# Optimization experiments

Hardware: AMD Instinct MI355X
Metric: run time of the kernel (lower is better)

The kernel has to match this reference:

```python
import jax, jax.numpy as jnp
import numpy as np

DILATIONS = [1, 2, 4, 8, 16, 32, 64, 128, 256, 512]
C = 256   # channels
K = 3     # kernel size


def causal_conv(x, w, b, d):
    # x: [B, C_in, T], w: [C_out, C_in, K] -> [B, C_out, T], left-padded causal
    y = jax.lax.conv_general_dilated(
        x, w,
        window_strides=(1,),
        padding=[((K - 1) * d, 0)],
        rhs_dilation=(d,),
        dimension_numbers=('NCH', 'OIH', 'NCH'))
    return y + b[None, :, None]


def setup_inputs() -> dict:
    key = jax.random.key(0)
    ks = jax.random.split(key, 5)
    L = len(DILATIONS)
    B, T = 4, 8192
    s = 0.05  # weight scale
    return {
        'input': jax.random.normal(ks[0], (B, C, T), jnp.float32),
        'weights_conv': jax.random.normal(ks[1], (L, 2 * C, C, K), jnp.float32) * s,
        'biases_conv': jax.random.normal(ks[2], (L, 2 * C), jnp.float32) * s,
        'weights_out': jax.random.normal(ks[3], (L, C, C), jnp.float32) * s,
        'biases_out': jax.random.normal(ks[4], (L, C), jnp.float32) * s,
    }


def reference(input, weights_conv, biases_conv, weights_out, biases_out):
    x = input  # [B, C, T]
    L = len(DILATIONS)
    skips = []
    for i, d in enumerate(DILATIONS):
        z = causal_conv(x, weights_conv[i], biases_conv[i], d)  # [B, 2C, T]
        # gated activation: tanh on first half, sigmoid on second half
        h = jnp.tanh(z[:, :C]) * jax.nn.sigmoid(z[:, C:])       # [B, C, T]
        skips.append(h)
        if i < L - 1:
            # 1x1 output transform (disabled on the last layer)
            out = jnp.einsum('oc,bct->bot', weights_out[i], h) + biases_out[i][None, :, None]
        else:
            out = h
        x = out + x  # residual connection applied in the stack
    return x, jnp.stack(skips, axis=0)  # ([B,C,T], [L,B,C,T])
```

## Files before the change

### kernel.cpp

```cpp
#include <hip/hip_runtime.h>
#include <hip/hip_bf16.h>

#define BATCH 4
#define CCH 256
#define TLEN 8192
#define LAYERS 10
#define BCT (BATCH*CCH*TLEN)
#define TPAD 1024
#define TROWS (TPAD + TLEN)

typedef __attribute__((ext_vector_type(8))) short bf16x8;
typedef __attribute__((ext_vector_type(4))) float f32x4;

__device__ __forceinline__ unsigned short f2b(float f) {
  union { float f; unsigned u; } v; v.f = f;
  unsigned r = (v.u + 0x7FFFu + ((v.u >> 16) & 1u)) >> 16;
  return (unsigned short)r;
}
__device__ __forceinline__ float b2f(unsigned short h) {
  union { unsigned u; float f; } v; v.u = ((unsigned)h) << 16;
  return v.f;
}

__device__ __forceinline__ void gload16(const void* g, void* l) {
  __builtin_amdgcn_global_load_lds((__attribute__((address_space(1))) void*)g,
                                   (__attribute__((address_space(3))) void*)l, 16, 0, 0);
}

__device__ __forceinline__ float fast_tanh(float x) {
  float a = fabsf(x);
  float e = __expf(-2.f * a);
  float th = (1.f - e) * __builtin_amdgcn_rcpf(1.f + e);
  return copysignf(th, x);
}
__device__ __forceinline__ float fast_sigmoid(float x) {
  return __builtin_amdgcn_rcpf(1.f + __expf(-x));
}

__global__ void repack_w(const float* __restrict__ wc, const float* __restrict__ wo,
                         unsigned short* __restrict__ Wb, unsigned short* __restrict__ Wob) {
  size_t g = (size_t)blockIdx.x * 256 + threadIdx.x;
  const size_t NA = (size_t)LAYERS * 3 * 4 * 128 * 256;
  if (g < NA) {
    int c   = (int)(g & 255);
    int row = (int)((g >> 8) & 127);
    int y   = (int)((g >> 15) & 3);
    int lt  = (int)(g >> 17);
    int tap = lt % 3, l = lt / 3;
    int ch = y * 64 + ((row >> 5) << 4) + (row & 15) + (((row >> 4) & 1) << 8);
    Wb[g] = f2b(wc[(((size_t)l * 512 + ch) * 256 + c) * 3 + tap]);
  } else {
    size_t g2 = g - NA;
    if (g2 < (size_t)LAYERS * 256 * 256) Wob[g2] = f2b(wo[g2]);
  }
}

__global__ void zero_pads(unsigned short* __restrict__ xTb) {
  size_t off = (size_t)blockIdx.y * TROWS * CCH;
  int i = blockIdx.x * 256 + threadIdx.x;
  ulonglong2 z; z.x = 0ull; z.y = 0ull;
  ((ulonglong2*)(xTb + off))[i] = z;
}

__global__ void transpose_in(const float* __restrict__ in, float* __restrict__ xT,
                             unsigned short* __restrict__ xTb) {
  __shared__ float tile[32][33];
  const int tid = threadIdx.x;
  const int t0 = blockIdx.x * 32, c0 = blockIdx.y * 32, b = blockIdx.z;
#pragma unroll
  for (int q = 0; q < 4; ++q) {
    int e = tid + 256 * q; int r = e >> 5, cc = e & 31;
    tile[r][cc] = in[((size_t)b * CCH + c0 + r) * TLEN + t0 + cc];
  }
  __syncthreads();
#pragma unroll
  for (int q = 0; q < 4; ++q) {
    int e = tid + 256 * q; int r = e >> 5, cc = e & 31;
    float v = tile[cc][r];
    xT[((size_t)b * TLEN + t0 + r) * CCH + c0 + cc] = v;
    xTb[((size_t)b * TROWS + TPAD + t0 + r) * CCH + c0 + cc] = f2b(v);
  }
}

__global__ void final_addT(const float* __restrict__ xT, const unsigned short* __restrict__ hT,
                           float* __restrict__ out) {
  __shared__ float tile[32][33];
  const int tid = threadIdx.x;
  const int t0 = blockIdx.x * 32, c0 = blockIdx.y * 32, b = blockIdx.z;
#pragma unroll
  for (int q = 0; q < 4; ++q) {
    int e = tid + 256 * q; int r = e >> 5, cc = e & 31;
    size_t idx = ((size_t)b * TLEN + t0 + r) * CCH + c0 + cc;
    tile[r][cc] = xT[idx] + b2f(hT[idx]);
  }
  __syncthreads();
#pragma unroll
  for (int q = 0; q < 4; ++q) {
    int e = tid + 256 * q; int r = e >> 5, cc = e & 31;
    out[((size_t)b * CCH + c0 + r) * TLEN + t0 + cc] = tile[cc][r];
  }
}

__global__ __launch_bounds__(256)
void conv_gate_kernel(const unsigned short* __restrict__ xTb,
                      const unsigned short* __restrict__ Wl,
                      const float* __restrict__ bias,
                      unsigned short* __restrict__ hT,
                      float* __restrict__ skip,
                      int d) {
  __shared__ unsigned short As[128 * 32];
  __shared__ unsigned short Bs[128 * 32];

  const int tid  = threadIdx.x;
  const int lane = tid & 63;
  const int wv   = tid >> 6;
  const int wm   = wv & 1, wn = wv >> 1;
  const int col  = lane & 15, quad = lane >> 4;

  const int t0 = blockIdx.x * 128;
  const int y  = blockIdx.y;
  const int o0 = y * 64;
  const int b  = blockIdx.z;

  const int rl = lane >> 2;
  const int kl = (lane & 3) * 8;
  const int ch0 = wv * 2;

  f32x4 acc[4][4];
  const f32x4 zero = {0.f, 0.f, 0.f, 0.f};
#pragma unroll
  for (int i = 0; i < 4; ++i)
#pragma unroll
    for (int j = 0; j < 4; ++j) acc[i][j] = zero;

  for (int tap = 0; tap < 3; ++tap) {
    const int s = (2 - tap) * d;
    const unsigned short* Ab = xTb + ((size_t)b * TROWS + TPAD + t0 - s) * CCH;
    const unsigned short* Wb = Wl + ((size_t)tap * 4 + y) * 128 * 256;
    for (int c0 = 0; c0 < 256; c0 += 32) {
      __syncthreads();
      gload16(Ab + (size_t)(ch0 * 16      + rl) * CCH + c0 + kl, &As[ ch0      * 512]);
      gload16(Ab + (size_t)(ch0 * 16 + 16 + rl) * CCH + c0 + kl, &As[(ch0 + 1) * 512]);
      gload16(Wb + (size_t)(ch0 * 16      + rl) * 256 + c0 + kl, &Bs[ ch0      * 512]);
      gload16(Wb + (size_t)(ch0 * 16 + 16 + rl) * 256 + c0 + kl, &Bs[(ch0 + 1) * 512]);
      __syncthreads();
      const int k0 = quad * 8;
      bf16x8 af[4], bfv[4];
#pragma unroll
      for (int mf = 0; mf < 4; ++mf)
        af[mf] = *(const bf16x8*)&As[(wm * 64 + mf * 16 + col) * 32 + k0];
#pragma unroll
      for (int nf = 0; nf < 4; ++nf)
        bfv[nf] = *(const bf16x8*)&Bs[(wn * 64 + nf * 16 + col) * 32 + k0];
#pragma unroll
      for (int mf = 0; mf < 4; ++mf)
#pragma unroll
        for (int nf = 0; nf < 4; ++nf)
          acc[mf][nf] = __builtin_amdgcn_mfma_f32_16x16x32_bf16(af[mf], bfv[nf], acc[mf][nf], 0, 0, 0);
    }
  }

#pragma unroll
  for (int mf = 0; mf < 4; ++mf) {
    const int tb = t0 + wm * 64 + mf * 16 + quad * 4;
#pragma unroll
    for (int p = 0; p < 2; ++p) {
      const int pair = wn * 2 + p;
      const int ch = o0 + pair * 16 + col;
      const float btop = bias[ch];
      const float bbot = bias[ch + 256];
      f32x4 zt = acc[mf][2 * p];
      f32x4 zb = acc[mf][2 * p + 1];
      float hr[4];
#pragma unroll
      for (int r = 0; r < 4; ++r) {
        float h = fast_tanh(zt[r] + btop) * fast_sigmoid(zb[r] + bbot);
        hr[r] = h;
        hT[((size_t)b * TLEN + tb + r) * CCH + ch] = f2b(h);
      }
      float4 hv; hv.x = hr[0]; hv.y = hr[1]; hv.z = hr[2]; hv.w = hr[3];
      *(float4*)&skip[((size_t)b * CCH + ch) * TLEN + tb] = hv;
    }
  }
}

__global__ __launch_bounds__(256)
void onexone_kernel(const unsigned short* __restrict__ hT,
                    const unsigned short* __restrict__ Wo,
                    const float* __restrict__ bias,
                    float* __restrict__ xT,
                    unsigned short* __restrict__ xTb) {
  __shared__ unsigned short As[128 * 32];
  __shared__ unsigned short Bs[128 * 32];

  const int tid  = threadIdx.x;
  const int lane = tid & 63;
  const int wv   = tid >> 6;
  const int wm   = wv & 1, wn = wv >> 1;
  const int col  = lane & 15, quad = lane >> 4;

  const int t0 = blockIdx.x * 128;
  const int o0 = blockIdx.y * 128;
  const int b  = blockIdx.z;

  const int rl = lane >> 2;
  const int kl = (lane & 3) * 8;
  const int ch0 = wv * 2;

  const unsigned short* Ab = hT + (size_t)b * TLEN * CCH + (size_t)t0 * CCH;
  const unsigned short* Wb = Wo + (size_t)o0 * 256;

  f32x4 acc[4][4];
  const f32x4 zero = {0.f, 0.f, 0.f, 0.f};
#pragma unroll
  for (int i = 0; i < 4; ++i)
#pragma unroll
    for (int j = 0; j < 4; ++j) acc[i][j] = zero;

  for (int c0 = 0; c0 < 256; c0 += 32) {
    __syncthreads();
    gload16(Ab + (size_t)(ch0 * 16      + rl) * CCH + c0 + kl, &As[ ch0      * 512]);
    gload16(Ab + (size_t)(ch0 * 16 + 16 + rl) * CCH + c0 + kl, &As[(ch0 + 1) * 512]);
    gload16(Wb + (size_t)(ch0 * 16      + rl) * 256 + c0 + kl, &Bs[ ch0      * 512]);
    gload16(Wb + (size_t)(ch0 * 16 + 16 + rl) * 256 + c0 + kl, &Bs[(ch0 + 1) * 512]);
    __syncthreads();
    const int k0 = quad * 8;
    bf16x8 af[4], bfv[4];
#pragma unroll
    for (int mf = 0; mf < 4; ++mf)
      af[mf] = *(const bf16x8*)&As[(wm * 64 + mf * 16 + col) * 32 + k0];
#pragma unroll
    for (int nf = 0; nf < 4; ++nf)
      bfv[nf] = *(const bf16x8*)&Bs[(wn * 64 + nf * 16 + col) * 32 + k0];
#pragma unroll
    for (int mf = 0; mf < 4; ++mf)
#pragma unroll
      for (int nf = 0; nf < 4; ++nf)
        acc[mf][nf] = __builtin_amdgcn_mfma_f32_16x16x32_bf16(af[mf], bfv[nf], acc[mf][nf], 0, 0, 0);
  }

#pragma unroll
  for (int mf = 0; mf < 4; ++mf) {
    const int tb = t0 + wm * 64 + mf * 16 + quad * 4;
#pragma unroll
    for (int nf = 0; nf < 4; ++nf) {
      const int ch = o0 + wn * 64 + nf * 16 + col;
      const float bo = bias[ch];
#pragma unroll
      for (int r = 0; r < 4; ++r) {
        size_t idx = ((size_t)b * TLEN + tb + r) * CCH + ch;
        float nv = xT[idx] + acc[mf][nf][r] + bo;
        xT[idx] = nv;
        xTb[((size_t)b * TROWS + TPAD + tb + r) * CCH + ch] = f2b(nv);
      }
    }
  }
}

extern "C" void kernel_launch(void* const* d_in, const int* in_sizes, int n_in,
                              void* d_out, int out_size, void* d_ws, size_t ws_size,
                              hipStream_t stream) {
  const float* input = (const float*)d_in[0];
  const float* wconv = (const float*)d_in[1];
  const float* bconv = (const float*)d_in[2];
  const float* wout  = (const float*)d_in[3];
  const float* bout  = (const float*)d_in[4];
  float* out   = (float*)d_out;
  float* skips = out + (size_t)BCT;

  char* ws = (char*)d_ws;
  float*          xT  = (float*)ws;
  unsigned short* xTb = (unsigned short*)(ws + (size_t)BCT * 4);
  unsigned short* hT  = (unsigned short*)(ws + (size_t)BCT * 4
                                             + (size_t)BATCH * TROWS * CCH * 2);
  unsigned short* Wb  = hT + (size_t)BCT;
  unsigned short* Wob = Wb + (size_t)LAYERS * 3 * 512 * 256;

  static const int dil[LAYERS] = {1, 2, 4, 8, 16, 32, 64, 128, 256, 512};

  repack_w<<<17920, 256, 0, stream>>>(wconv, wout, Wb, Wob);
  zero_pads<<<dim3(128, BATCH), 256, 0, stream>>>(xTb);
  transpose_in<<<dim3(TLEN / 32, CCH / 32, BATCH), 256, 0, stream>>>(input, xT, xTb);

  for (int l = 0; l < LAYERS; ++l) {
    conv_gate_kernel<<<dim3(TLEN / 128, 4, BATCH), 256, 0, stream>>>(
        xTb, Wb + (size_t)l * 3 * 512 * 256, bconv + (size_t)l * 512,
        hT, skips + (size_t)l * BCT, dil[l]);
    if (l < LAYERS - 1) {
      onexone_kernel<<<dim3(TLEN / 128, 2, BATCH), 256, 0, stream>>>(
          hT, Wob + (size_t)l * 256 * 256, bout + (size_t)l * 256, xT, xTb);
    } else {
      final_addT<<<dim3(TLEN / 32, CCH / 32, BATCH), 256, 0, stream>>>(xT, hT, out);
    }
  }
}
```

Before: 1.045 ms.

## Double-buffer LDS tiles in conv and 1x1 GEMM kernels

Both the dilated-conv gate kernel and the 1x1 output kernel now use two LDS buffers. The next K-chunk is issued (flattened over taps and channel chunks) while MFMAs run on the current one, which removes one barrier per iteration. This is meant to hide global-to-LDS load latency behind compute. In exchange, LDS use per block doubles, which may reduce occupancy, and whether the overlap happens depends on how gload16 completes.

```diff
diff --git a/kernel.cpp b/kernel.cpp
--- a/kernel.cpp
+++ b/kernel.cpp
@@ -108,8 +108,8 @@
                       unsigned short* __restrict__ hT,
                       float* __restrict__ skip,
                       int d) {
-  __shared__ unsigned short As[128 * 32];
-  __shared__ unsigned short Bs[128 * 32];
+  __shared__ unsigned short As[2][128 * 32];
+  __shared__ unsigned short Bs[2][128 * 32];
 
   const int tid  = threadIdx.x;
   const int lane = tid & 63;
@@ -126,6 +126,8 @@
   const int kl = (lane & 3) * 8;
   const int ch0 = wv * 2;
 
+  const unsigned short* Arow = xTb + ((size_t)b * TROWS + TPAD + t0) * CCH;
+
   f32x4 acc[4][4];
   const f32x4 zero = {0.f, 0.f, 0.f, 0.f};
 #pragma unroll
@@ -133,31 +135,42 @@
 #pragma unroll
     for (int j = 0; j < 4; ++j) acc[i][j] = zero;
 
-  for (int tap = 0; tap < 3; ++tap) {
-    const int s = (2 - tap) * d;
-    const unsigned short* Ab = xTb + ((size_t)b * TROWS + TPAD + t0 - s) * CCH;
-    const unsigned short* Wb = Wl + ((size_t)tap * 4 + y) * 128 * 256;
-    for (int c0 = 0; c0 < 256; c0 += 32) {
-      __syncthreads();
-      gload16(Ab + (size_t)(ch0 * 16      + rl) * CCH + c0 + kl, &As[ ch0      * 512]);
-      gload16(Ab + (size_t)(ch0 * 16 + 16 + rl) * CCH + c0 + kl, &As[(ch0 + 1) * 512]);
-      gload16(Wb + (size_t)(ch0 * 16      + rl) * 256 + c0 + kl, &Bs[ ch0      * 512]);
-      gload16(Wb + (size_t)(ch0 * 16 + 16 + rl) * 256 + c0 + kl, &Bs[(ch0 + 1) * 512]);
-      __syncthreads();
-      const int k0 = quad * 8;
-      bf16x8 af[4], bfv[4];
-#pragma unroll
-      for (int mf = 0; mf < 4; ++mf)
-        af[mf] = *(const bf16x8*)&As[(wm * 64 + mf * 16 + col) * 32 + k0];
+  const int NCHUNK = 24;
+
+  auto stage = [&](int idx, int buf) {
+    const int tap = idx >> 3;
+    const int c0  = (idx & 7) << 5;
+    const unsigned short* Ab = Arow - (size_t)((2 - tap) * d) * CCH;
+    const unsigned short* Wb = Wl + ((size_t)tap * 4 + y) * (128 * 256);
+    gload16(Ab + (size_t)(ch0 * 16      + rl) * CCH + c0 + kl, &As[buf][ ch0      * 512]);
+    gload16(Ab + (size_t)(ch0 * 16 + 16 + rl) * CCH + c0 + kl, &As[buf][(ch0 + 1) * 512]);
+    gload16(Wb + (size_t)(ch0 * 16      + rl) * 256 + c0 + kl, &Bs[buf][ ch0      * 512]);
+    gload16(Wb + (size_t)(ch0 * 16 + 16 + rl) * 256 + c0 + kl, &Bs[buf][(ch0 + 1) * 512]);
+  };
+
+  auto step = [&](int buf, int next_idx) {
+    const int k0 = quad * 8;
+    bf16x8 af[4], bfv[4];
+#pragma unroll
+    for (int mf = 0; mf < 4; ++mf)
+      af[mf] = *(const bf16x8*)&As[buf][(wm * 64 + mf * 16 + col) * 32 + k0];
+#pragma unroll
+    for (int nf = 0; nf < 4; ++nf)
+      bfv[nf] = *(const bf16x8*)&Bs[buf][(wn * 64 + nf * 16 + col) * 32 + k0];
+    if (next_idx < NCHUNK) stage(next_idx, buf ^ 1);
+#pragma unroll
+    for (int mf = 0; mf < 4; ++mf)
 #pragma unroll
       for (int nf = 0; nf < 4; ++nf)
-        bfv[nf] = *(const bf16x8*)&Bs[(wn * 64 + nf * 16 + col) * 32 + k0];
-#pragma unroll
-      for (int mf = 0; mf < 4; ++mf)
-#pragma unroll
-        for (int nf = 0; nf < 4; ++nf)
-          acc[mf][nf] = __builtin_amdgcn_mfma_f32_16x16x32_bf16(af[mf], bfv[nf], acc[mf][nf], 0, 0, 0);
-    }
+        acc[mf][nf] = __builtin_amdgcn_mfma_f32_16x16x32_bf16(af[mf], bfv[nf], acc[mf][nf], 0, 0, 0);
+  };
+
+  stage(0, 0);
+  __syncthreads();
+#pragma unroll 1
+  for (int i = 0; i < NCHUNK; i += 2) {
+    step(0, i + 1); __syncthreads();
+    step(1, i + 2); __syncthreads();
   }
 
 #pragma unroll
@@ -190,8 +203,8 @@
                     const float* __restrict__ bias,
                     float* __restrict__ xT,
                     unsigned short* __restrict__ xTb) {
-  __shared__ unsigned short As[128 * 32];
-  __shared__ unsigned short Bs[128 * 32];
+  __shared__ unsigned short As[2][128 * 32];
+  __shared__ unsigned short Bs[2][128 * 32];
 
   const int tid  = threadIdx.x;
   const int lane = tid & 63;
@@ -217,26 +230,39 @@
 #pragma unroll
     for (int j = 0; j < 4; ++j) acc[i][j] = zero;
 
-  for (int c0 = 0; c0 < 256; c0 += 32) {
-    __syncthreads();
-    gload16(Ab + (size_t)(ch0 * 16      + rl) * CCH + c0 + kl, &As[ ch0      * 512]);
-    gload16(Ab + (size_t)(ch0 * 16 + 16 + rl) * CCH + c0 + kl, &As[(ch0 + 1) * 512]);
-    gload16(Wb + (size_t)(ch0 * 16      + rl) * 256 + c0 + kl, &Bs[ ch0      * 512]);
-    gload16(Wb + (size_t)(ch0 * 16 + 16 + rl) * 256 + c0 + kl, &Bs[(ch0 + 1) * 512]);
-    __syncthreads();
+  const int NCHUNK = 8;
+
+  auto stage = [&](int idx, int buf) {
+    const int c0 = idx << 5;
+    gload16(Ab + (size_t)(ch0 * 16      + rl) * CCH + c0 + kl, &As[buf][ ch0      * 512]);
+    gload16(Ab + (size_t)(ch0 * 16 + 16 + rl) * CCH + c0 + kl, &As[buf][(ch0 + 1) * 512]);
+    gload16(Wb + (size_t)(ch0 * 16      + rl) * 256 + c0 + kl, &Bs[buf][ ch0      * 512]);
+    gload16(Wb + (size_t)(ch0 * 16 + 16 + rl) * 256 + c0 + kl, &Bs[buf][(ch0 + 1) * 512]);
+  };
+
+  auto step = [&](int buf, int next_idx) {
     const int k0 = quad * 8;
     bf16x8 af[4], bfv[4];
 #pragma unroll
     for (int mf = 0; mf < 4; ++mf)
-      af[mf] = *(const bf16x8*)&As[(wm * 64 + mf * 16 + col) * 32 + k0];
+      af[mf] = *(const bf16x8*)&As[buf][(wm * 64 + mf * 16 + col) * 32 + k0];
 #pragma unroll
     for (int nf = 0; nf < 4; ++nf)
-      bfv[nf] = *(const bf16x8*)&Bs[(wn * 64 + nf * 16 + col) * 32 + k0];
+      bfv[nf] = *(const bf16x8*)&Bs[buf][(wn * 64 + nf * 16 + col) * 32 + k0];
+    if (next_idx < NCHUNK) stage(next_idx, buf ^ 1);
 #pragma unroll
     for (int mf = 0; mf < 4; ++mf)
 #pragma unroll
       for (int nf = 0; nf < 4; ++nf)
         acc[mf][nf] = __builtin_amdgcn_mfma_f32_16x16x32_bf16(af[mf], bfv[nf], acc[mf][nf], 0, 0, 0);
+  };
+
+  stage(0, 0);
+  __syncthreads();
+#pragma unroll 1
+  for (int i = 0; i < NCHUNK; i += 2) {
+    step(0, i + 1); __syncthreads();
+    step(1, i + 2); __syncthreads();
   }
 
 #pragma unroll
```

Result: no change. 1.061 ms (+1.6%).
